# Kernel optimization log

Measured on AMD Instinct MI355X. Metric: run time of the kernel, lower is better.

Reference implementation:

```python
import jax, jax.numpy as jnp
import numpy as np

def setup_inputs() -> dict:
    key = jax.random.key(0)
    ks = jax.random.split(key, 6)
    ch, cr = 256, 32  # cr = ch // 8
    B, H, W = 4, 64, 64
    sc = 1.0 / np.sqrt(ch)
    return {
        "inputs": jax.random.normal(ks[0], (B, H, W, ch), jnp.float32),
        "Wf": jax.random.normal(ks[1], (ch, cr), jnp.float32) * sc,
        "bf": jnp.zeros((cr,), jnp.float32),
        "Wg": jax.random.normal(ks[2], (ch, cr), jnp.float32) * sc,
        "bg": jnp.zeros((cr,), jnp.float32),
        "Wh": jax.random.normal(ks[3], (ch, cr), jnp.float32) * sc,
        "bh": jnp.zeros((cr,), jnp.float32),
        "Wv": jax.random.normal(ks[4], (cr, ch), jnp.float32) * (1.0 / np.sqrt(cr)),
        "bv": jnp.zeros((ch,), jnp.float32),
        "gamma": jnp.zeros((1,), jnp.float32),
    }

def reference(inputs, Wf, bf, Wg, bg, Wh, bh, Wv, bv, gamma):
    B, H, W, C = inputs.shape
    x = inputs.reshape(B, H * W, C)  # [B, N, C]
    f = x @ Wf + bf  # [B, N, cr] (keys)
    g = x @ Wg + bg  # [B, N, cr] (queries)
    h = x @ Wh + bh  # [B, N, cr] (values)
    s = jnp.einsum('bnk,bmk->bnm', g, f)  # [B, N, N]
    beta = jax.nn.softmax(s, axis=-1)
    v = jnp.einsum('bnm,bmk->bnk', beta, h)  # [B, N, cr]
    o = v @ Wv + bv  # [B, N, C]
    out = gamma * o + x
    return out.reshape(B, H, W, C)
```

## Files before the change

### kernel.cpp

```cpp
#include <hip/hip_runtime.h>

#define B_SZ  4
#define N_TOK 4096
#define CH    256
#define CR    32
#define SEG   256
#define KT    32
#define NITER (SEG / KT)
#define LOG2E 1.44269504f

typedef __attribute__((ext_vector_type(8))) short bf16x8;
typedef __attribute__((ext_vector_type(4))) float f32x4;

__device__ inline ushort f2bf(float x) {
    uint u = __float_as_uint(x);
    u += 0x7fff + ((u >> 16) & 1);
    return (ushort)(u >> 16);
}
__device__ inline uint pk2bf(float a, float b) {
    return __builtin_amdgcn_perm(__float_as_uint(b), __float_as_uint(a), 0x07060302);
}
__device__ inline float fast_exp2(float x) {
#if __has_builtin(__builtin_amdgcn_exp2f)
    return __builtin_amdgcn_exp2f(x);
#else
    return exp2f(x);
#endif
}

__device__ inline float exp_pack_row(const f32x4 s0, const f32x4 s1, ushort* rp, int Q) {
    float p0 = fast_exp2(s0[0]), p1 = fast_exp2(s0[1]);
    float p2 = fast_exp2(s0[2]), p3 = fast_exp2(s0[3]);
    float s4 = ((p0 + p1) + (p2 + p3));
    uint2 w; w.x = pk2bf(p0, p1); w.y = pk2bf(p2, p3);
    *(uint2*)(rp + Q * 4) = w;
    p0 = fast_exp2(s1[0]); p1 = fast_exp2(s1[1]);
    p2 = fast_exp2(s1[2]); p3 = fast_exp2(s1[3]);
    s4 += ((p0 + p1) + (p2 + p3));
    w.x = pk2bf(p0, p1); w.y = pk2bf(p2, p3);
    *(uint2*)(rp + 16 + Q * 4) = w;
    return s4;
}

__global__ __launch_bounds__(256) void proj_kernel(
    const float* __restrict__ x,
    const float* __restrict__ Wf, const float* __restrict__ Wg, const float* __restrict__ Wh,
    const float* __restrict__ bf_, const float* __restrict__ bg, const float* __restrict__ bh,
    ushort* __restrict__ fo, ushort* __restrict__ go, ushort* __restrict__ hto)
{
    __shared__ ushort wst[3][32][264];
    int t = threadIdx.x;

    {
        float4 r4[8];
        const float* rf = (const float*)&r4[0];
        #pragma unroll
        for (int q4 = 0; q4 < 8; ++q4) r4[q4] = *(const float4*)(Wf + (size_t)t * CR + q4 * 4);
        #pragma unroll
        for (int j = 0; j < 32; ++j) wst[0][j][t] = f2bf(rf[j]);
        #pragma unroll
        for (int q4 = 0; q4 < 8; ++q4) r4[q4] = *(const float4*)(Wg + (size_t)t * CR + q4 * 4);
        #pragma unroll
        for (int j = 0; j < 32; ++j) wst[1][j][t] = f2bf(rf[j]);
        #pragma unroll
        for (int q4 = 0; q4 < 8; ++q4) r4[q4] = *(const float4*)(Wh + (size_t)t * CR + q4 * 4);
        #pragma unroll
        for (int j = 0; j < 32; ++j) wst[2][j][t] = f2bf(rf[j]);
    }
    __syncthreads();

    int wv = t >> 6, L = t & 63, nl = L & 15, Q = L >> 4;
    int row_t = blockIdx.x * 64 + wv * 16;
    int b = row_t >> 12, tok0 = row_t & 4095;

    const float* xrow = x + (size_t)(row_t + nl) * CH;
    f32x4 A[6];
    #pragma unroll
    for (int i = 0; i < 6; ++i) A[i] = (f32x4){0.f, 0.f, 0.f, 0.f};

    #pragma unroll
    for (int kk = 0; kk < 8; ++kk) {
        int off = kk * 32 + Q * 8;
        float4 lo = *(const float4*)(xrow + off);
        float4 hi = *(const float4*)(xrow + off + 4);
        bf16x8 xa;
        xa[0] = (short)f2bf(lo.x); xa[1] = (short)f2bf(lo.y);
        xa[2] = (short)f2bf(lo.z); xa[3] = (short)f2bf(lo.w);
        xa[4] = (short)f2bf(hi.x); xa[5] = (short)f2bf(hi.y);
        xa[6] = (short)f2bf(hi.z); xa[7] = (short)f2bf(hi.w);

        bf16x8 wf0 = *(const bf16x8*)&wst[0][nl][off];
        bf16x8 wf1 = *(const bf16x8*)&wst[0][16 + nl][off];
        bf16x8 wg0 = *(const bf16x8*)&wst[1][nl][off];
        bf16x8 wg1 = *(const bf16x8*)&wst[1][16 + nl][off];
        bf16x8 wh0 = *(const bf16x8*)&wst[2][nl][off];
        bf16x8 wh1 = *(const bf16x8*)&wst[2][16 + nl][off];

        A[0] = __builtin_amdgcn_mfma_f32_16x16x32_bf16(xa, wf0, A[0], 0, 0, 0);
        A[1] = __builtin_amdgcn_mfma_f32_16x16x32_bf16(xa, wf1, A[1], 0, 0, 0);
        A[2] = __builtin_amdgcn_mfma_f32_16x16x32_bf16(xa, wg0, A[2], 0, 0, 0);
        A[3] = __builtin_amdgcn_mfma_f32_16x16x32_bf16(xa, wg1, A[3], 0, 0, 0);
        A[4] = __builtin_amdgcn_mfma_f32_16x16x32_bf16(wh0, xa, A[4], 0, 0, 0);
        A[5] = __builtin_amdgcn_mfma_f32_16x16x32_bf16(wh1, xa, A[5], 0, 0, 0);
    }

    float bF0 = bf_[nl], bF1 = bf_[16 + nl];
    float bG0 = bg[nl] * LOG2E, bG1 = bg[16 + nl] * LOG2E;
    #pragma unroll
    for (int r = 0; r < 4; ++r) {
        size_t ro = (size_t)(row_t + Q * 4 + r) * CR;
        fo[ro + nl]      = f2bf(A[0][r] + bF0);
        fo[ro + 16 + nl] = f2bf(A[1][r] + bF1);
        go[ro + nl]      = f2bf(fmaf(A[2][r], LOG2E, bG0));
        go[ro + 16 + nl] = f2bf(fmaf(A[3][r], LOG2E, bG1));
    }
    ushort* hb = hto + (size_t)b * CR * N_TOK + (size_t)(tok0 >> 5) * (CR * 32) + (tok0 & 31) + nl;
    #pragma unroll
    for (int r = 0; r < 4; ++r) {
        int ch = Q * 4 + r;
        hb[ch * 32]        = f2bf(A[4][r] + bh[ch]);
        hb[(16 + ch) * 32] = f2bf(A[5][r] + bh[16 + ch]);
    }
}

__global__ __launch_bounds__(1024, 4) void attn_kernel(
    const ushort* __restrict__ f, const ushort* __restrict__ g,
    const ushort* __restrict__ ht, const float* __restrict__ Wv,
    const float* __restrict__ bv, const float* __restrict__ gamma,
    const float* __restrict__ x, float* __restrict__ out)
{
    __shared__ unsigned long long smem_raw[81920 / 8];
    ushort (*pls)[64][40]  = (ushort (*)[64][40])smem_raw;
    float  (*obuf)[64][33] = (float (*)[64][33])smem_raw;
    float  (*lbuf)[64]     = (float (*)[64])((char*)smem_raw + 67584);
    ushort (*oc)[48]       = (ushort (*)[48])((char*)smem_raw + 71680);

    int t  = threadIdx.x;
    int wv = t >> 6;
    int L  = t & 63;
    int nl = L & 15;
    int Q  = L >> 4;
    int bid = blockIdx.x;
    int swz = (bid & 7) * 32 + (bid >> 3);
    int b  = swz >> 6;
    int q0 = (swz & 63) * 64;

    const ushort* fb  = f  + (size_t)b * N_TOK * CR;
    const ushort* htb = ht + (size_t)b * CR * N_TOK;

    bf16x8 gB[4];
    #pragma unroll
    for (int qh = 0; qh < 4; ++qh)
        gB[qh] = *(const bf16x8*)(g + ((size_t)b * N_TOK + q0 + qh * 16 + nl) * CR + Q * 8);

    f32x4 acc[4][2];
    #pragma unroll
    for (int i = 0; i < 4; ++i) { acc[i][0] = (f32x4){0,0,0,0}; acc[i][1] = (f32x4){0,0,0,0}; }
    const f32x4 zf = {0,0,0,0};
    float ls0 = 0.f, ls1 = 0.f, ls2 = 0.f, ls3 = 0.f;

    int key0 = wv * SEG;
    bf16x8 Ac0 = *(const bf16x8*)(fb + (size_t)(key0 +      nl) * CR + Q * 8);
    bf16x8 Ac1 = *(const bf16x8*)(fb + (size_t)(key0 + 16 + nl) * CR + Q * 8);

    #pragma unroll 2
    for (int it = 0; it < NITER; ++it) {
        int kc = key0 + it * KT;
        const ushort* hk = htb + (size_t)kc * CR + nl * 32 + Q * 8;
        bf16x8 bh0 = *(const bf16x8*)(hk);
        bf16x8 bh1 = *(const bf16x8*)(hk + 512);
        int kn = key0 + ((it + 1 < NITER) ? it + 1 : 0) * KT;
        bf16x8 An0 = *(const bf16x8*)(fb + (size_t)(kn +      nl) * CR + Q * 8);
        bf16x8 An1 = *(const bf16x8*)(fb + (size_t)(kn + 16 + nl) * CR + Q * 8);

        f32x4 t0, t1;
        t0 = __builtin_amdgcn_mfma_f32_16x16x32_bf16(Ac0, gB[0], zf, 0, 0, 0);
        t1 = __builtin_amdgcn_mfma_f32_16x16x32_bf16(Ac1, gB[0], zf, 0, 0, 0);
        ls0 += exp_pack_row(t0, t1, &pls[wv][nl][0], Q);
        t0 = __builtin_amdgcn_mfma_f32_16x16x32_bf16(Ac0, gB[1], zf, 0, 0, 0);
        t1 = __builtin_amdgcn_mfma_f32_16x16x32_bf16(Ac1, gB[1], zf, 0, 0, 0);
        ls1 += exp_pack_row(t0, t1, &pls[wv][16 + nl][0], Q);
        bf16x8 aP0 = *(const bf16x8*)&pls[wv][     nl][Q * 8];
        bf16x8 aP1 = *(const bf16x8*)&pls[wv][16 + nl][Q * 8];
        t0 = __builtin_amdgcn_mfma_f32_16x16x32_bf16(Ac0, gB[2], zf, 0, 0, 0);
        t1 = __builtin_amdgcn_mfma_f32_16x16x32_bf16(Ac1, gB[2], zf, 0, 0, 0);
        ls2 += exp_pack_row(t0, t1, &pls[wv][32 + nl][0], Q);
        bf16x8 aP2 = *(const bf16x8*)&pls[wv][32 + nl][Q * 8];
        __builtin_amdgcn_s_setprio(1);
        acc[0][0] = __builtin_amdgcn_mfma_f32_16x16x32_bf16(aP0, bh0, acc[0][0], 0, 0, 0);
        acc[0][1] = __builtin_amdgcn_mfma_f32_16x16x32_bf16(aP0, bh1, acc[0][1], 0, 0, 0);
        acc[1][0] = __builtin_amdgcn_mfma_f32_16x16x32_bf16(aP1, bh0, acc[1][0], 0, 0, 0);
        acc[1][1] = __builtin_amdgcn_mfma_f32_16x16x32_bf16(aP1, bh1, acc[1][1], 0, 0, 0);
        __builtin_amdgcn_s_setprio(0);
        t0 = __builtin_amdgcn_mfma_f32_16x16x32_bf16(Ac0, gB[3], zf, 0, 0, 0);
        t1 = __builtin_amdgcn_mfma_f32_16x16x32_bf16(Ac1, gB[3], zf, 0, 0, 0);
        ls3 += exp_pack_row(t0, t1, &pls[wv][48 + nl][0], Q);
        bf16x8 aP3 = *(const bf16x8*)&pls[wv][48 + nl][Q * 8];
        __builtin_amdgcn_s_setprio(1);
        acc[2][0] = __builtin_amdgcn_mfma_f32_16x16x32_bf16(aP2, bh0, acc[2][0], 0, 0, 0);
        acc[2][1] = __builtin_amdgcn_mfma_f32_16x16x32_bf16(aP2, bh1, acc[2][1], 0, 0, 0);
        acc[3][0] = __builtin_amdgcn_mfma_f32_16x16x32_bf16(aP3, bh0, acc[3][0], 0, 0, 0);
        acc[3][1] = __builtin_amdgcn_mfma_f32_16x16x32_bf16(aP3, bh1, acc[3][1], 0, 0, 0);
        __builtin_amdgcn_s_setprio(0);

        Ac0 = An0; Ac1 = An1;
    }

    ls0 += __shfl_xor(ls0, 16); ls0 += __shfl_xor(ls0, 32);
    ls1 += __shfl_xor(ls1, 16); ls1 += __shfl_xor(ls1, 32);
    ls2 += __shfl_xor(ls2, 16); ls2 += __shfl_xor(ls2, 32);
    ls3 += __shfl_xor(ls3, 16); ls3 += __shfl_xor(ls3, 32);

    __syncthreads();

    if (wv >= 8) {
        #pragma unroll
        for (int qh = 0; qh < 4; ++qh)
            #pragma unroll
            for (int r = 0; r < 4; ++r) {
                obuf[wv - 8][qh * 16 + Q * 4 + r][nl]      = acc[qh][0][r];
                obuf[wv - 8][qh * 16 + Q * 4 + r][16 + nl] = acc[qh][1][r];
            }
    }
    if (L < 16) {
        lbuf[wv][     nl] = ls0; lbuf[wv][16 + nl] = ls1;
        lbuf[wv][32 + nl] = ls2; lbuf[wv][48 + nl] = ls3;
    }
    __syncthreads();
    if (wv < 8) {
        #pragma unroll
        for (int qh = 0; qh < 4; ++qh)
            #pragma unroll
            for (int r = 0; r < 4; ++r) {
                obuf[wv][qh * 16 + Q * 4 + r][nl]      += acc[qh][0][r];
                obuf[wv][qh * 16 + Q * 4 + r][16 + nl] += acc[qh][1][r];
            }
    }
    __syncthreads();

    {
        int ch = t & 31, qb = t >> 5;
        #pragma unroll
        for (int qq = qb; qq < 64; qq += 32) {
            float s = 0.f, Lq = 0.f;
            #pragma unroll
            for (int w = 0; w < 8; ++w) s += obuf[w][qq][ch];
            #pragma unroll
            for (int w = 0; w < 16; ++w) Lq += lbuf[w][qq];
            oc[qq][ch] = f2bf(s / Lq);
        }
    }
    __syncthreads();

    float gm = gamma[0];
    const float* xb = x   + ((size_t)b * N_TOK + q0) * CH;
    float*       ob = out + ((size_t)b * N_TOK + q0) * CH;
    int c = wv * 16 + nl;
    const float* wvp = Wv + c;
    bf16x8 bW;
    #pragma unroll
    for (int j = 0; j < 8; ++j) bW[j] = (short)f2bf(wvp[(size_t)(Q * 8 + j) * CH]);
    float bvc = bv[c];
    #pragma unroll
    for (int qg = 0; qg < 4; ++qg) {
        bf16x8 aO = *(const bf16x8*)&oc[qg * 16 + nl][Q * 8];
        f32x4 d = __builtin_amdgcn_mfma_f32_16x16x32_bf16(aO, bW, zf, 0, 0, 0);
        #pragma unroll
        for (int r = 0; r < 4; ++r) {
            int qa = qg * 16 + Q * 4 + r;
            ob[qa * CH + c] = fmaf(gm, d[r] + bvc, xb[qa * CH + c]);
        }
    }
}

extern "C" void kernel_launch(void* const* d_in, const int* in_sizes, int n_in,
                              void* d_out, int out_size, void* d_ws, size_t ws_size,
                              hipStream_t stream) {
    const float* x     = (const float*)d_in[0];
    const float* Wf    = (const float*)d_in[1];
    const float* bf_   = (const float*)d_in[2];
    const float* Wg    = (const float*)d_in[3];
    const float* bg    = (const float*)d_in[4];
    const float* Wh    = (const float*)d_in[5];
    const float* bh    = (const float*)d_in[6];
    const float* Wv    = (const float*)d_in[7];
    const float* bv    = (const float*)d_in[8];
    const float* gamma = (const float*)d_in[9];
    float* out = (float*)d_out;

    const size_t T = (size_t)B_SZ * N_TOK * CR;
    ushort* fo  = (ushort*)d_ws;
    ushort* go  = fo + T;
    ushort* hto = go + T;

    proj_kernel<<<B_SZ * N_TOK / 64, 256, 0, stream>>>(x, Wf, Wg, Wh, bf_, bg, bh, fo, go, hto);
    attn_kernel<<<B_SZ * (N_TOK / 64), 1024, 0, stream>>>(fo, go, hto, Wv, bv, gamma, x, out);
}
```

Before: 112.4 us.

## Split projection K-reduction across two wave groups and coalesce output epilogue via LDS

The projection kernel now runs 512 threads per block. Two wave groups each handle half of the 256-channel reduction, and their partial MFMA accumulators are combined through shared memory before the bf16 outputs are written. Separately, the attention kernel's final Wv projection stages its results in LDS, so the residual add reads x and writes out with row-contiguous float4 accesses instead of scattered scalar stores. The aim is more parallelism and latency hiding in the projection and coalesced global traffic in the epilogue. The cost is an extra barrier and LDS round trip in each kernel.

```diff
diff --git a/kernel.cpp b/kernel.cpp
--- a/kernel.cpp
+++ b/kernel.cpp
@@ -42,35 +42,38 @@
     return s4;
 }
 
-__global__ __launch_bounds__(256) void proj_kernel(
+__global__ __launch_bounds__(512) void proj_kernel(
     const float* __restrict__ x,
     const float* __restrict__ Wf, const float* __restrict__ Wg, const float* __restrict__ Wh,
     const float* __restrict__ bf_, const float* __restrict__ bg, const float* __restrict__ bh,
     ushort* __restrict__ fo, ushort* __restrict__ go, ushort* __restrict__ hto)
 {
     __shared__ ushort wst[3][32][264];
+    __shared__ f32x4 cmb[4][6][64];
     int t = threadIdx.x;
 
     {
-        float4 r4[8];
+        int krow = t & 255, j0 = (t >> 8) << 4;
+        float4 r4[4];
         const float* rf = (const float*)&r4[0];
         #pragma unroll
-        for (int q4 = 0; q4 < 8; ++q4) r4[q4] = *(const float4*)(Wf + (size_t)t * CR + q4 * 4);
-        #pragma unroll
-        for (int j = 0; j < 32; ++j) wst[0][j][t] = f2bf(rf[j]);
-        #pragma unroll
-        for (int q4 = 0; q4 < 8; ++q4) r4[q4] = *(const float4*)(Wg + (size_t)t * CR + q4 * 4);
-        #pragma unroll
-        for (int j = 0; j < 32; ++j) wst[1][j][t] = f2bf(rf[j]);
-        #pragma unroll
-        for (int q4 = 0; q4 < 8; ++q4) r4[q4] = *(const float4*)(Wh + (size_t)t * CR + q4 * 4);
-        #pragma unroll
-        for (int j = 0; j < 32; ++j) wst[2][j][t] = f2bf(rf[j]);
+        for (int q4 = 0; q4 < 4; ++q4) r4[q4] = *(const float4*)(Wf + (size_t)krow * CR + j0 + q4 * 4);
+        #pragma unroll
+        for (int jj = 0; jj < 16; ++jj) wst[0][j0 + jj][krow] = f2bf(rf[jj]);
+        #pragma unroll
+        for (int q4 = 0; q4 < 4; ++q4) r4[q4] = *(const float4*)(Wg + (size_t)krow * CR + j0 + q4 * 4);
+        #pragma unroll
+        for (int jj = 0; jj < 16; ++jj) wst[1][j0 + jj][krow] = f2bf(rf[jj]);
+        #pragma unroll
+        for (int q4 = 0; q4 < 4; ++q4) r4[q4] = *(const float4*)(Wh + (size_t)krow * CR + j0 + q4 * 4);
+        #pragma unroll
+        for (int jj = 0; jj < 16; ++jj) wst[2][j0 + jj][krow] = f2bf(rf[jj]);
     }
     __syncthreads();
 
     int wv = t >> 6, L = t & 63, nl = L & 15, Q = L >> 4;
-    int row_t = blockIdx.x * 64 + wv * 16;
+    int tw = wv & 3, kh = wv >> 2;
+    int row_t = blockIdx.x * 64 + tw * 16;
     int b = row_t >> 12, tok0 = row_t & 4095;
 
     const float* xrow = x + (size_t)(row_t + nl) * CH;
@@ -79,8 +82,8 @@
     for (int i = 0; i < 6; ++i) A[i] = (f32x4){0.f, 0.f, 0.f, 0.f};
 
     #pragma unroll
-    for (int kk = 0; kk < 8; ++kk) {
-        int off = kk * 32 + Q * 8;
+    for (int k2 = 0; k2 < 4; ++k2) {
+        int off = (kh * 4 + k2) * 32 + Q * 8;
         float4 lo = *(const float4*)(xrow + off);
         float4 hi = *(const float4*)(xrow + off + 4);
         bf16x8 xa;
@@ -104,22 +107,32 @@
         A[5] = __builtin_amdgcn_mfma_f32_16x16x32_bf16(wh1, xa, A[5], 0, 0, 0);
     }
 
-    float bF0 = bf_[nl], bF1 = bf_[16 + nl];
-    float bG0 = bg[nl] * LOG2E, bG1 = bg[16 + nl] * LOG2E;
-    #pragma unroll
-    for (int r = 0; r < 4; ++r) {
-        size_t ro = (size_t)(row_t + Q * 4 + r) * CR;
-        fo[ro + nl]      = f2bf(A[0][r] + bF0);
-        fo[ro + 16 + nl] = f2bf(A[1][r] + bF1);
-        go[ro + nl]      = f2bf(fmaf(A[2][r], LOG2E, bG0));
-        go[ro + 16 + nl] = f2bf(fmaf(A[3][r], LOG2E, bG1));
-    }
-    ushort* hb = hto + (size_t)b * CR * N_TOK + (size_t)(tok0 >> 5) * (CR * 32) + (tok0 & 31) + nl;
-    #pragma unroll
-    for (int r = 0; r < 4; ++r) {
-        int ch = Q * 4 + r;
-        hb[ch * 32]        = f2bf(A[4][r] + bh[ch]);
-        hb[(16 + ch) * 32] = f2bf(A[5][r] + bh[16 + ch]);
+    if (kh) {
+        #pragma unroll
+        for (int i = 0; i < 6; ++i) cmb[tw][i][L] = A[i];
+    }
+    __syncthreads();
+    if (!kh) {
+        #pragma unroll
+        for (int i = 0; i < 6; ++i) A[i] = A[i] + cmb[tw][i][L];
+
+        float bF0 = bf_[nl], bF1 = bf_[16 + nl];
+        float bG0 = bg[nl] * LOG2E, bG1 = bg[16 + nl] * LOG2E;
+        #pragma unroll
+        for (int r = 0; r < 4; ++r) {
+            size_t ro = (size_t)(row_t + Q * 4 + r) * CR;
+            fo[ro + nl]      = f2bf(A[0][r] + bF0);
+            fo[ro + 16 + nl] = f2bf(A[1][r] + bF1);
+            go[ro + nl]      = f2bf(fmaf(A[2][r], LOG2E, bG0));
+            go[ro + 16 + nl] = f2bf(fmaf(A[3][r], LOG2E, bG1));
+        }
+        ushort* hb = hto + (size_t)b * CR * N_TOK + (size_t)(tok0 >> 5) * (CR * 32) + (tok0 & 31) + nl;
+        #pragma unroll
+        for (int r = 0; r < 4; ++r) {
+            int ch = Q * 4 + r;
+            hb[ch * 32]        = f2bf(A[4][r] + bh[ch]);
+            hb[(16 + ch) * 32] = f2bf(A[5][r] + bh[16 + ch]);
+        }
     }
 }
 
@@ -134,6 +147,7 @@
     float  (*obuf)[64][33] = (float (*)[64][33])smem_raw;
     float  (*lbuf)[64]     = (float (*)[64])((char*)smem_raw + 67584);
     ushort (*oc)[48]       = (ushort (*)[48])((char*)smem_raw + 71680);
+    float  (*ofs)[264]     = (float (*)[264])smem_raw;
 
     int t  = threadIdx.x;
     int wv = t >> 6;
@@ -253,22 +267,41 @@
     __syncthreads();
 
     float gm = gamma[0];
-    const float* xb = x   + ((size_t)b * N_TOK + q0) * CH;
-    float*       ob = out + ((size_t)b * N_TOK + q0) * CH;
     int c = wv * 16 + nl;
     const float* wvp = Wv + c;
     bf16x8 bW;
     #pragma unroll
     for (int j = 0; j < 8; ++j) bW[j] = (short)f2bf(wvp[(size_t)(Q * 8 + j) * CH]);
     float bvc = bv[c];
+    f32x4 dq[4];
     #pragma unroll
     for (int qg = 0; qg < 4; ++qg) {
         bf16x8 aO = *(const bf16x8*)&oc[qg * 16 + nl][Q * 8];
-        f32x4 d = __builtin_amdgcn_mfma_f32_16x16x32_bf16(aO, bW, zf, 0, 0, 0);
-        #pragma unroll
-        for (int r = 0; r < 4; ++r) {
-            int qa = qg * 16 + Q * 4 + r;
-            ob[qa * CH + c] = fmaf(gm, d[r] + bvc, xb[qa * CH + c]);
+        dq[qg] = __builtin_amdgcn_mfma_f32_16x16x32_bf16(aO, bW, zf, 0, 0, 0);
+    }
+    #pragma unroll
+    for (int qg = 0; qg < 4; ++qg)
+        #pragma unroll
+        for (int r = 0; r < 4; ++r)
+            ofs[qg * 16 + Q * 4 + r][c] = dq[qg][r] + bvc;
+    __syncthreads();
+
+    {
+        int q  = t >> 4;
+        int i4 = (t & 15) * 4;
+        const float* xrow = x   + ((size_t)b * N_TOK + q0 + q) * CH;
+        float*       orow = out + ((size_t)b * N_TOK + q0 + q) * CH;
+        #pragma unroll
+        for (int j = 0; j < 4; ++j) {
+            int col = i4 + j * 64;
+            f32x4 v = *(const f32x4*)&ofs[q][col];
+            float4 xv = *(const float4*)(xrow + col);
+            float4 o;
+            o.x = fmaf(gm, v[0], xv.x);
+            o.y = fmaf(gm, v[1], xv.y);
+            o.z = fmaf(gm, v[2], xv.z);
+            o.w = fmaf(gm, v[3], xv.w);
+            *(float4*)(orow + col) = o;
         }
     }
 }
@@ -293,6 +326,6 @@
     ushort* go  = fo + T;
     ushort* hto = go + T;
 
-    proj_kernel<<<B_SZ * N_TOK / 64, 256, 0, stream>>>(x, Wf, Wg, Wh, bf_, bg, bh, fo, go, hto);
+    proj_kernel<<<B_SZ * N_TOK / 64, 512, 0, stream>>>(x, Wf, Wg, Wh, bf_, bg, bh, fo, go, hto);
     attn_kernel<<<B_SZ * (N_TOK / 64), 1024, 0, stream>>>(fo, go, hto, Wv, bv, gamma, x, out);
 }
```

After: 114.1 us. No clear change (+1.5%).
